# Performance work log

Hardware: AMD Instinct MI355X
Metric: run time of the kernel (lower is better)

Reference implementation:

```python
import jax, jax.numpy as jnp
import numpy as np

GROUP_SIZE = 128


def _unpack_int4(packed):
    # packed: [..., P] int32, each holding 8 int4 nibbles (LSB-first).
    u = jax.lax.bitcast_convert_type(packed, jnp.uint32)
    shifts = jnp.arange(8, dtype=jnp.uint32) * 4  # nibble bit offsets
    vals = (u[..., None] >> shifts) & jnp.uint32(15)  # [..., P, 8]
    return vals.reshape(*packed.shape[:-1], -1)  # [..., P*8] in [0, 15]


def setup_inputs() -> dict:
    key = jax.random.key(0)
    k1, k2, k3, k4 = jax.random.split(key, 4)
    B, S, K, O = 4, 16, 4096, 11008
    G = K // GROUP_SIZE          # 32 groups
    GP = (G + 7) // 8            # 4 packed-zero columns
    imax = np.iinfo(np.int32).max
    x = jax.random.normal(k1, (B, S, K), dtype=jnp.float16)
    qweight_i32 = jax.random.randint(k2, (O, K // 8), 0, imax, dtype=jnp.int32)
    qzeros_i32 = jax.random.randint(k3, (O, GP), 0, imax, dtype=jnp.int32)
    scales_f16 = jax.random.uniform(k4, (O, G), dtype=jnp.float16,
                                    minval=0.001, maxval=0.02)
    return {"x": x, "qweight_i32": qweight_i32, "qzeros_i32": qzeros_i32,
            "scales_f16": scales_f16}


def reference(x, qweight_i32, qzeros_i32, scales_f16):
    O, G = scales_f16.shape
    K = G * GROUP_SIZE
    # Dequantize: w = (q - z) * s, per-group int4 quantization.
    q = _unpack_int4(qweight_i32)[:, :K].astype(jnp.float16)       # [O, K]
    z = _unpack_int4(qzeros_i32)[:, :G].astype(jnp.float16)        # [O, G]
    z_k = jnp.repeat(z, GROUP_SIZE, axis=1)                        # [O, K]
    s_k = jnp.repeat(scales_f16, GROUP_SIZE, axis=1)               # [O, K]
    w = (q - z_k) * s_k                                            # fp16 [O, K]
    x2d = x.reshape(-1, K).astype(jnp.float16)                     # [m, K]
    out = jnp.matmul(x2d, w.T).astype(jnp.float32)                 # [m, O]
    return out.reshape(*x.shape[:-1], O)
```

## Files before the change

### kernel.cpp

```cpp
#include <hip/hip_runtime.h>
#include <stdint.h>

typedef _Float16 half8   __attribute__((ext_vector_type(8)));
typedef float    floatx4 __attribute__((ext_vector_type(4)));
typedef float    floatx16 __attribute__((ext_vector_type(16)));
typedef uint32_t uint4v  __attribute__((ext_vector_type(4)));

#define KDIM 4096
#define ODIM 11008
#define NG   32

__global__ void zero_out_kernel(float4* __restrict__ out) {
    out[(size_t)blockIdx.x * 256 + threadIdx.x] = float4{0.f, 0.f, 0.f, 0.f};
}

__device__ __forceinline__ uint32_t pk_f16(float a, float b) {
    return __builtin_bit_cast(uint32_t, __builtin_amdgcn_cvt_pkrtz(a, b));
}

__device__ __forceinline__ half8 dq(uint32_t ud) {
    const uint4v bw = {
        ( ud         & 0x000F000Fu) | 0x64006400u,
        ((ud >> 4)   & 0x000F000Fu) | 0x64006400u,
        ((ud >> 8)   & 0x000F000Fu) | 0x64006400u,
        ((ud >> 12)  & 0x000F000Fu) | 0x64006400u};
    return __builtin_bit_cast(half8, bw);
}

__global__ __launch_bounds__(256) void cvt_x_kernel(
    const float4* __restrict__ x, uint4v* __restrict__ xh3,
    float* __restrict__ xsumT)
{
    const int i = blockIdx.x * 256 + threadIdx.x;
    const float4 f0 = x[2 * i];
    const float4 f1 = x[2 * i + 1];
    const uint4v v = {pk_f16(f0.x, f1.x), pk_f16(f0.y, f1.y),
                      pk_f16(f0.z, f1.z), pk_f16(f0.w, f1.w)};
    const int m  = i >> 9, c = i & 511;
    const int g  = c >> 4, cg = c & 15, h = cg >> 3, ks = cg & 7;
    const int mt = m >> 5, ml = m & 31;
    xh3[((size_t)(g * 8 + ks) * 2 + mt) * 64 + h * 32 + ml] = v;

    float p = f0.x + f0.y + f0.z + f0.w + f1.x + f1.y + f1.z + f1.w;
    p += __shfl_xor(p, 1);
    p += __shfl_xor(p, 2);
    p += __shfl_xor(p, 4);
    p += __shfl_xor(p, 8);
    if ((threadIdx.x & 15) == 0) xsumT[g * 64 + m] = p;
}

__global__ __launch_bounds__(256, 2) void w4a16_kernel(
    const uint4v*   __restrict__ xh3,
    const uint4v*   __restrict__ qw,
    const uint32_t* __restrict__ qz,
    const float*    __restrict__ sc,
    const float*    __restrict__ xsumT,
    float*          __restrict__ out)
{
    __shared__ float red[4][2048];

    const int t    = threadIdx.x;
    const int kw   = t >> 6;
    const int lane = t & 63;
    const int h    = lane >> 5;
    const int ml   = lane & 31;

    const int kb = blockIdx.x & 1;
    const int ob = blockIdx.x >> 1;
    const int o0 = ob * 32;
    const int o  = o0 + ml;
    const int g0 = kb * 16 + kw * 4;

    const uint4v* qwp = qw + (size_t)o * 128 + g0 * 4 + h * 2;
    const uint32_t zdw = qz[(size_t)o * 4 + (g0 >> 3)];
    const int zsh = (g0 & 7) * 4;
    const floatx4 sv = *reinterpret_cast<const floatx4*>(sc + (size_t)o * NG + g0);

    const uint4v* xp = xh3 + (size_t)g0 * 16 * 64 + lane;

    floatx16 acc[2] = {};

    uint4v u0 = qwp[0], u1 = qwp[1];

    #pragma unroll 1
    for (int gi = 0; gi < 4; ++gi) {
        const uint4v c0 = u0, c1 = u1;
        if (gi + 1 < 4) { u0 = qwp[(gi + 1) * 4]; u1 = qwp[(gi + 1) * 4 + 1]; }

        const int   g   = g0 + gi;
        const float s   = sv[gi];
        const uint32_t zn = (zdw >> (zsh + gi * 4)) & 0xFu;
        const float czs = s * (1024.0f + (float)zn);

        half8 b[8];
        #pragma unroll
        for (int ks = 0; ks < 4; ++ks) { b[ks] = dq(c0[ks]); b[4 + ks] = dq(c1[ks]); }

        #pragma unroll
        for (int mt = 0; mt < 2; ++mt) {
            uint4v ax[8];
            #pragma unroll
            for (int ks = 0; ks < 8; ++ks)
                ax[ks] = xp[(size_t)(gi * 16 + ks * 2 + mt) * 64];

            floatx16 tmp = {};
            #pragma unroll
            for (int ks = 0; ks < 8; ++ks)
                tmp = __builtin_amdgcn_mfma_f32_32x32x16_f16(
                    __builtin_bit_cast(half8, ax[ks]), b[ks], tmp, 0, 0, 0);

            #pragma unroll
            for (int rr = 0; rr < 4; ++rr) {
                const floatx4 xsg = *reinterpret_cast<const floatx4*>(
                    xsumT + g * 64 + mt * 32 + rr * 8 + h * 4);
                #pragma unroll
                for (int j = 0; j < 4; ++j)
                    acc[mt][rr * 4 + j] += s * tmp[rr * 4 + j] - czs * xsg[j];
            }
        }
    }

    #pragma unroll
    for (int mt = 0; mt < 2; ++mt)
        #pragma unroll
        for (int rr = 0; rr < 4; ++rr)
            #pragma unroll
            for (int j = 0; j < 4; ++j) {
                const int m = mt * 32 + rr * 8 + h * 4 + j;
                red[kw][m * 32 + ml] = acc[mt][rr * 4 + j];
            }
    __syncthreads();

    #pragma unroll
    for (int r = 0; r < 8; ++r) {
        const int i  = r * 256 + t;
        const int m  = i >> 5, ol = i & 31;
        const float v = red[0][i] + red[1][i] + red[2][i] + red[3][i];
        atomicAdd(out + (size_t)m * ODIM + o0 + ol, v);
    }
}

extern "C" void kernel_launch(void* const* d_in, const int* in_sizes, int n_in,
                              void* d_out, int out_size, void* d_ws, size_t ws_size,
                              hipStream_t stream) {
    const float*    x       = (const float*)d_in[0];
    const uint32_t* qweight = (const uint32_t*)d_in[1];
    const uint32_t* qzeros  = (const uint32_t*)d_in[2];
    const float*    scales  = (const float*)d_in[3];
    float* out = (float*)d_out;

    uint4v* xh3   = (uint4v*)d_ws;
    float*  xsumT = (float*)((char*)d_ws + 512 * 1024);

    cvt_x_kernel<<<dim3(128), dim3(256), 0, stream>>>((const float4*)x, xh3, xsumT);
    zero_out_kernel<<<dim3(688), dim3(256), 0, stream>>>((float4*)out);
    w4a16_kernel<<<dim3(688), dim3(256), 0, stream>>>(
        xh3, (const uint4v*)qweight, qzeros, scales, xsumT, out);
}
```

Before: 93.98 us.

## Split M tiles across waves and quadruple K-split blocks for more occupancy

Each wave now handles a single 32-row M tile instead of both, and the K dimension is split four ways across blocks instead of two, so the grid grows to 1376 blocks. This lowers per-wave register and LDS use and allows four blocks per CU. The cost is that each weight tile is dequantized and loaded by two waves instead of one, and twice as many atomicAdds reach the output.

```diff
diff --git a/kernel.cpp b/kernel.cpp
--- a/kernel.cpp
+++ b/kernel.cpp
@@ -49,7 +49,7 @@
     if ((threadIdx.x & 15) == 0) xsumT[g * 64 + m] = p;
 }
 
-__global__ __launch_bounds__(256, 2) void w4a16_kernel(
+__global__ __launch_bounds__(256, 4) void w4a16_kernel(
     const uint4v*   __restrict__ xh3,
     const uint4v*   __restrict__ qw,
     const uint32_t* __restrict__ qz,
@@ -57,28 +57,30 @@
     const float*    __restrict__ xsumT,
     float*          __restrict__ out)
 {
-    __shared__ float red[4][2048];
+    __shared__ float red[2][2048];
 
     const int t    = threadIdx.x;
-    const int kw   = t >> 6;
+    const int wv   = t >> 6;
+    const int mt   = wv & 1;
+    const int ks2  = wv >> 1;
     const int lane = t & 63;
     const int h    = lane >> 5;
     const int ml   = lane & 31;
 
-    const int kb = blockIdx.x & 1;
-    const int ob = blockIdx.x >> 1;
+    const int kb = blockIdx.x & 3;
+    const int ob = blockIdx.x >> 2;
     const int o0 = ob * 32;
     const int o  = o0 + ml;
-    const int g0 = kb * 16 + kw * 4;
+    const int g0 = kb * 8 + ks2 * 4;
 
     const uint4v* qwp = qw + (size_t)o * 128 + g0 * 4 + h * 2;
     const uint32_t zdw = qz[(size_t)o * 4 + (g0 >> 3)];
     const int zsh = (g0 & 7) * 4;
     const floatx4 sv = *reinterpret_cast<const floatx4*>(sc + (size_t)o * NG + g0);
 
-    const uint4v* xp = xh3 + (size_t)g0 * 16 * 64 + lane;
+    const uint4v* xp = xh3 + ((size_t)g0 * 16 + mt) * 64 + lane;
 
-    floatx16 acc[2] = {};
+    floatx16 acc = {};
 
     uint4v u0 = qwp[0], u1 = qwp[1];
 
@@ -92,50 +94,45 @@
         const uint32_t zn = (zdw >> (zsh + gi * 4)) & 0xFu;
         const float czs = s * (1024.0f + (float)zn);
 
-        half8 b[8];
+        uint4v ax[8];
         #pragma unroll
-        for (int ks = 0; ks < 4; ++ks) { b[ks] = dq(c0[ks]); b[4 + ks] = dq(c1[ks]); }
+        for (int ks = 0; ks < 8; ++ks)
+            ax[ks] = xp[(size_t)(gi * 16 + ks * 2) * 64];
+
+        floatx16 tmp = {};
+        #pragma unroll
+        for (int ks = 0; ks < 4; ++ks)
+            tmp = __builtin_amdgcn_mfma_f32_32x32x16_f16(
+                __builtin_bit_cast(half8, ax[ks]), dq(c0[ks]), tmp, 0, 0, 0);
+        #pragma unroll
+        for (int ks = 0; ks < 4; ++ks)
+            tmp = __builtin_amdgcn_mfma_f32_32x32x16_f16(
+                __builtin_bit_cast(half8, ax[4 + ks]), dq(c1[ks]), tmp, 0, 0, 0);
 
         #pragma unroll
-        for (int mt = 0; mt < 2; ++mt) {
-            uint4v ax[8];
+        for (int rr = 0; rr < 4; ++rr) {
+            const floatx4 xsg = *reinterpret_cast<const floatx4*>(
+                xsumT + g * 64 + mt * 32 + rr * 8 + h * 4);
             #pragma unroll
-            for (int ks = 0; ks < 8; ++ks)
-                ax[ks] = xp[(size_t)(gi * 16 + ks * 2 + mt) * 64];
-
-            floatx16 tmp = {};
-            #pragma unroll
-            for (int ks = 0; ks < 8; ++ks)
-                tmp = __builtin_amdgcn_mfma_f32_32x32x16_f16(
-                    __builtin_bit_cast(half8, ax[ks]), b[ks], tmp, 0, 0, 0);
-
-            #pragma unroll
-            for (int rr = 0; rr < 4; ++rr) {
-                const floatx4 xsg = *reinterpret_cast<const floatx4*>(
-                    xsumT + g * 64 + mt * 32 + rr * 8 + h * 4);
-                #pragma unroll
-                for (int j = 0; j < 4; ++j)
-                    acc[mt][rr * 4 + j] += s * tmp[rr * 4 + j] - czs * xsg[j];
-            }
+            for (int j = 0; j < 4; ++j)
+                acc[rr * 4 + j] += s * tmp[rr * 4 + j] - czs * xsg[j];
         }
     }
 
     #pragma unroll
-    for (int mt = 0; mt < 2; ++mt)
+    for (int rr = 0; rr < 4; ++rr)
         #pragma unroll
-        for (int rr = 0; rr < 4; ++rr)
-            #pragma unroll
-            for (int j = 0; j < 4; ++j) {
-                const int m = mt * 32 + rr * 8 + h * 4 + j;
-                red[kw][m * 32 + ml] = acc[mt][rr * 4 + j];
-            }
+        for (int j = 0; j < 4; ++j) {
+            const int m = rr * 8 + h * 4 + j;
+            red[ks2][mt * 1024 + m * 32 + ml] = acc[rr * 4 + j];
+        }
     __syncthreads();
 
     #pragma unroll
     for (int r = 0; r < 8; ++r) {
-        const int i  = r * 256 + t;
-        const int m  = i >> 5, ol = i & 31;
-        const float v = red[0][i] + red[1][i] + red[2][i] + red[3][i];
+        const int i = r * 256 + t;
+        const int m = i >> 5, ol = i & 31;
+        const float v = red[0][i] + red[1][i];
         atomicAdd(out + (size_t)m * ODIM + o0 + ol, v);
     }
 }
@@ -154,6 +151,6 @@
 
     cvt_x_kernel<<<dim3(128), dim3(256), 0, stream>>>((const float4*)x, xh3, xsumT);
     zero_out_kernel<<<dim3(688), dim3(256), 0, stream>>>((float4*)out);
-    w4a16_kernel<<<dim3(688), dim3(256), 0, stream>>>(
+    w4a16_kernel<<<dim3(344 * 4), dim3(256), 0, stream>>>(
         xh3, (const uint4v*)qweight, qzeros, scales, xsumT, out);
 }
```

Result: slower. 100.3 us (+6.8%).
